# Kernel tuning notes

Hardware: AMD Instinct MI355X
Metric: run time of the kernel (lower is better)

## Reference

```python
import jax, jax.numpy as jnp
import numpy as np

EPS = 1e-6
T = 10.0
STEPS = 3
BN_EPS = 1e-5

def _normalize(x, axis):
    n = jnp.sqrt(jnp.sum(x * x, axis=axis, keepdims=True))
    return x / jnp.maximum(n, EPS)

def _vq_step(X, D):
    # X: (B, d, n), D: (B, d, r)
    Dn = _normalize(D, 1)
    Xn = _normalize(X, 1)
    cos = jnp.einsum('bdr,bdn->brn', Dn, Xn)          # (B, r, n)
    C = jax.nn.softmax(cos / T, axis=1)               # softmax over r
    XCt = jnp.einsum('bdn,brn->bdr', X, C)            # (B, d, r)
    sums = jnp.maximum(jnp.sum(C, axis=2), EPS)       # (B, r)
    D2 = _normalize(XCt / sums[:, None, :], 1)
    Xbar = jnp.einsum('bdr,brn->bdn', D2, C)
    return D2, C, Xbar

def _ham_vq(X, D0):
    # K-1 steps without gradient tracking, final step with grad through X only
    Xs = jax.lax.stop_gradient(X)
    def body(D, _):
        D, _, _ = _vq_step(Xs, D)
        return D, None
    D, _ = jax.lax.scan(body, _normalize(D0, 1), None, length=STEPS - 1)
    D = jax.lax.stop_gradient(D)
    _, _, Xbar = _vq_step(X, D)
    return Xbar

def _conv1x1(x, w, b=None):
    y = jnp.einsum('oc,bchw->bohw', w, x)
    if b is not None:
        y = y + b[None, :, None, None]
    return y

def _bn(x, gamma, beta, mean, var):
    inv = gamma / jnp.sqrt(var + BN_EPS)
    return x * inv[None, :, None, None] + (beta - mean * inv)[None, :, None, None]


def setup_inputs() -> dict:
    key = jax.random.key(0)
    ks = jax.random.split(key, 16)
    B, Cin, H, W = 8, 512, 64, 64
    d_mid, r = 512, 64
    out_ch = 2 * d_mid  # dual
    sc = 0.02
    inp = {
        'z': jax.random.normal(ks[0], (B, Cin, H, W), jnp.float32),
        'lower_w': jax.random.normal(ks[1], (out_ch, Cin), jnp.float32) * sc,
        'lower_b': jnp.zeros((out_ch,), jnp.float32),
        'Dinit_s': jax.random.uniform(ks[2], (B, d_mid, r), jnp.float32),
        'Dinit_c': jax.random.uniform(ks[3], (B, d_mid, r), jnp.float32),
        'cheese_w': jax.random.normal(ks[4], (out_ch, out_ch), jnp.float32) * sc,
        'ch_gamma': jnp.ones((out_ch,), jnp.float32),
        'ch_beta': jnp.zeros((out_ch,), jnp.float32),
        'ch_mean': jax.random.normal(ks[5], (out_ch,), jnp.float32) * 0.1,
        'ch_var': jax.random.uniform(ks[6], (out_ch,), jnp.float32) + 0.5,
        'upper_w': jax.random.normal(ks[7], (Cin, out_ch), jnp.float32) * sc,
        'upper_b': jnp.zeros((Cin,), jnp.float32),
        'h_gamma': jnp.ones((Cin,), jnp.float32),
        'h_beta': jnp.zeros((Cin,), jnp.float32),
        'h_mean': jax.random.normal(ks[8], (Cin,), jnp.float32) * 0.1,
        'h_var': jax.random.uniform(ks[9], (Cin,), jnp.float32) + 0.5,
        'coef_ham': jnp.array(1.0, jnp.float32),
        'coef_shortcut': jnp.array(1.0, jnp.float32),
    }
    return inp


def reference(z, lower_w, lower_b, Dinit_s, Dinit_c, cheese_w,
              ch_gamma, ch_beta, ch_mean, ch_var, upper_w, upper_b,
              h_gamma, h_beta, h_mean, h_var, coef_ham, coef_shortcut):
    B, Cin, H, W = z.shape
    identity = z
    # lower: conv1x1 + relu
    y = jax.nn.relu(_conv1x1(z, lower_w, lower_b))       # (B, 2*d_mid, H, W)
    d_mid = y.shape[1] // 2
    y1, y2 = y[:, :d_mid], y[:, d_mid:]
    n = H * W
    # spatial ham
    Xs = y1.reshape(B, d_mid, n)
    y1 = _ham_vq(Xs, Dinit_s).reshape(B, d_mid, H, W)
    # channel ham (same (B, d, n) flattening; HamMD requires dim1 == d_mid)
    Xc = y2.reshape(B, d_mid, n)
    y2 = _ham_vq(Xc, Dinit_c).reshape(B, d_mid, H, W)
    y = jnp.concatenate([y1, y2], axis=1)
    # cheese: conv1x1(no bias) + BN + relu
    y = jax.nn.relu(_bn(_conv1x1(y, cheese_w), ch_gamma, ch_beta, ch_mean, ch_var))
    # upper conv1x1 + BN
    h = _bn(_conv1x1(y, upper_w, upper_b), h_gamma, h_beta, h_mean, h_var)
    out = coef_ham * h + coef_shortcut * identity
    return jax.nn.relu(out)
```

## Files before the change

kernel.cpp:

```cpp
#include <hip/hip_runtime.h>
#include <hip/hip_bf16.h>

typedef __bf16 bf16_t;
typedef __bf16 bf16x4 __attribute__((ext_vector_type(4)));
typedef __bf16 bf16x8 __attribute__((ext_vector_type(8)));
typedef float  f32x4  __attribute__((ext_vector_type(4)));

#define HEPS 1e-6f

__device__ __forceinline__ void gload16(const bf16_t* g, bf16_t* l) {
    __builtin_amdgcn_global_load_lds(
        (const __attribute__((address_space(1))) unsigned int*)(g),
        (__attribute__((address_space(3))) unsigned int*)(l),
        16, 0, 0);
}


__global__ void cvt_f32_bf16_k(const float* __restrict__ src, bf16_t* __restrict__ dst, int n) {
    int i = blockIdx.x * 256 + threadIdx.x;
    if (i < n) dst[i] = (bf16_t)src[i];
}

__global__ void prep_k(const float* __restrict__ chg, const float* __restrict__ chb,
                       const float* __restrict__ chm, const float* __restrict__ chv,
                       const float* __restrict__ hg, const float* __restrict__ hb,
                       const float* __restrict__ hm, const float* __restrict__ hv,
                       const float* __restrict__ ub, const float* __restrict__ cham,
                       float* __restrict__ chA, float* __restrict__ chB,
                       float* __restrict__ hA2, float* __restrict__ hB2) {
    int i = blockIdx.x * 256 + threadIdx.x;
    if (i < 1024) {
        float inv = chg[i] * rsqrtf(chv[i] + 1e-5f);
        chA[i] = inv;
        chB[i] = chb[i] - chm[i] * inv;
    }
    if (i < 512) {
        float inv = hg[i] * rsqrtf(hv[i] + 1e-5f);
        float cA = cham[0];
        hA2[i] = cA * inv;
        hB2[i] = cA * (fmaf(ub[i], inv, hb[i]) - hm[i] * inv);
    }
}

__global__ void tz_k(const float* __restrict__ z, bf16_t* __restrict__ Zt) {
    __shared__ bf16_t t[64][68];
    int b = blockIdx.z, kt = blockIdx.y, nt = blockIdx.x;
    const float* src = z + ((size_t)b * 512 + kt * 64) * 4096 + nt * 64;
    int tid = threadIdx.x;
    int kr = tid >> 4;
    int nc = (tid & 15) * 4;
    #pragma unroll
    for (int it = 0; it < 4; ++it) {
        int k = kr + it * 16;
        float4 v = *(const float4*)&src[(size_t)k * 4096 + nc];
        t[nc + 0][k] = (bf16_t)v.x; t[nc + 1][k] = (bf16_t)v.y;
        t[nc + 2][k] = (bf16_t)v.z; t[nc + 3][k] = (bf16_t)v.w;
    }
    __syncthreads();
    bf16_t* dst = Zt + ((size_t)b * 4096 + nt * 64) * 512 + kt * 64;
    int nr = tid >> 4;
    int kc = (tid & 15) * 4;
    #pragma unroll
    for (int it = 0; it < 4; ++it) {
        int n = nr + it * 16;
        bf16x4 o;
        #pragma unroll
        for (int c = 0; c < 4; ++c) o[c] = t[n][kc + c];
        *(bf16x4*)&dst[(size_t)n * 512 + kc] = o;
    }
}

__global__ void dinit_k(const float* __restrict__ Ds, const float* __restrict__ Dc,
                        bf16_t* __restrict__ Dt) {
    int bs = blockIdx.y;
    int b = bs >> 1;
    const float* src = ((bs & 1) ? Dc : Ds) + (size_t)b * 512 * 64;
    int idx = blockIdx.x * 256 + threadIdx.x;
    int r = idx & 63, d = idx >> 6;
    Dt[(size_t)bs * 64 * 512 + (size_t)r * 512 + d] = (bf16_t)src[d * 64 + r];
}

__global__ void xnorm2_k(const bf16_t* __restrict__ Xt, float* __restrict__ xinv) {
    int gid = blockIdx.x * 4 + (threadIdx.x >> 6);
    int lane = threadIdx.x & 63;
    int bs = gid >> 12, n = gid & 4095;
    const bf16_t* row = Xt + ((size_t)(bs >> 1) * 4096 + n) * 1024 + (bs & 1) * 512 + lane * 8;
    bf16x8 v = *(const bf16x8*)row;
    float s = 0.f;
    #pragma unroll
    for (int e = 0; e < 8; ++e) { float f = (float)v[e]; s += f * f; }
    #pragma unroll
    for (int off = 32; off > 0; off >>= 1) s += __shfl_xor(s, off);
    if (lane == 0) xinv[gid] = 1.0f / (10.0f * fmaxf(sqrtf(s), HEPS));
}

__global__ void dnorm_k(const bf16_t* __restrict__ Dt, float* __restrict__ dinv) {
    int gw = (blockIdx.x * 256 + threadIdx.x) >> 6;
    int lane = threadIdx.x & 63;
    bf16x8 v = *(const bf16x8*)(Dt + (size_t)gw * 512 + lane * 8);
    float s = 0.f;
    #pragma unroll
    for (int e = 0; e < 8; ++e) { float f = (float)v[e]; s += f * f; }
    #pragma unroll
    for (int off = 32; off > 0; off >>= 1) s += __shfl_xor(s, off);
    if (lane == 0) dinv[gw] = 1.0f / fmaxf(sqrtf(s), HEPS);
}

__global__ void reduce_k(const float* __restrict__ P, bf16_t* __restrict__ Dt,
                         float* __restrict__ dinv) {
    int bsr = blockIdx.x;
    int bs = bsr >> 6, r = bsr & 63;
    int lane = threadIdx.x;
    const float* base = P + ((size_t)(bs * 4) * 64 + r) * 512 + lane * 8;
    float s[8] = {0.f, 0.f, 0.f, 0.f, 0.f, 0.f, 0.f, 0.f};
    #pragma unroll
    for (int kc = 0; kc < 4; ++kc) {
        const float* p = base + (size_t)kc * 64 * 512;
        float4 u = *(const float4*)p;
        float4 w = *(const float4*)(p + 4);
        s[0] += u.x; s[1] += u.y; s[2] += u.z; s[3] += u.w;
        s[4] += w.x; s[5] += w.y; s[6] += w.z; s[7] += w.w;
    }
    bf16x8 o;
    float sq = 0.f;
    #pragma unroll
    for (int e = 0; e < 8; ++e) { sq += s[e] * s[e]; o[e] = (bf16_t)s[e]; }
    *(bf16x8*)&Dt[(size_t)bsr * 512 + lane * 8] = o;
    #pragma unroll
    for (int off = 32; off > 0; off >>= 1) sq += __shfl_xor(sq, off);
    if (lane == 0) dinv[bsr] = 1.0f / fmaxf(sqrtf(sq), HEPS);
}

template<int BM, int BN, int WAVES_M, int WAVES_N, int EPI, int ORDER>
__launch_bounds__(256)
__global__ void g2(const bf16_t* __restrict__ Ag, const bf16_t* __restrict__ Bg,
                   void* __restrict__ Cg, void* __restrict__ C2g,
                   const int M, const int N, const int K,
                   const int ldA, const int ldB, const int ldC,
                   const long aStride, const long bStride,
                   const long cStride, const long c2Stride,
                   const float* __restrict__ p0, const float* __restrict__ p1,
                   const float* __restrict__ scal,
                   const float* __restrict__ shortcut, const long sStride)
{
    constexpr int WM = BM / WAVES_M, WN = BN / WAVES_N;
    constexpr int FM = WM / 16, FN = WN / 16;
    constexpr int ASEG = BM / 64, BSEG = BN / 64;
    constexpr int LPT = ASEG + BSEG;

    __shared__ __align__(64) bf16_t SH[3 * (BM + BN) * 32];
    __shared__ float dl[64];
    bf16_t* Al = SH;
    bf16_t* Bl = SH + 3 * BM * 32;

    const int tid = threadIdx.x;
    const int wave = tid >> 6, lane = tid & 63;
    const int l15 = lane & 15, q = lane >> 4;
    const int lrow = lane >> 2, lcol = (lane & 3) * 8;

    const int gx = gridDim.x, gy = gridDim.y;
    const int per = gx * gy;
    const int nwg = per * gridDim.z;
    const int g = blockIdx.z * per + blockIdx.y * gx + blockIdx.x;
    const int qq = nwg >> 3, rr = nwg & 7;
    const int xcd = g & 7, jj = g >> 3;
    const int w = (xcd < rr ? xcd * (qq + 1) : rr * (qq + 1) + (xcd - rr) * qq) + jj;
    const int bz = w / per;
    const int rem = w - bz * per;
    int bx, by;
    if constexpr (ORDER == 0) { by = rem / gx; bx = rem - by * gx; }
    else                      { bx = rem / gy; by = rem - bx * gy; }

    int bs = bz, exA = 0, exB = 0;
    if constexpr (EPI == 5) { bs = bz >> 2; exA = exB = (bz & 3) * 1024; }
    if constexpr (EPI == 7) { exA = (bz & 1) * 512; }

    const int n0 = bx * BN;
    const int m0 = by * BM;
    const int wm0 = (wave / WAVES_N) * WM;
    const int wn0 = (wave % WAVES_N) * WN;

    const bf16_t* Ab = Ag + (size_t)bs * (size_t)aStride + exA;
    const bf16_t* Bb;
    if constexpr (EPI == 6)
        Bb = Bg + (size_t)(bz >> 1) * (size_t)bStride + (size_t)(bz & 1) * 512;
    else
        Bb = Bg + (size_t)bs * (size_t)bStride + exB;

    if constexpr (EPI == 6) { if (tid < 64) dl[tid] = p0[bz * 64 + tid]; }

    auto stage = [&](int buf, int k0) {
        #pragma unroll
        for (int t = 0; t < ASEG; ++t) {
            int seg = wave * ASEG + t;
            gload16(Ab + (size_t)(m0 + seg * 16 + lrow) * ldA + k0 + lcol,
                    &Al[buf * BM * 32 + seg * 512]);
        }
        #pragma unroll
        for (int t = 0; t < BSEG; ++t) {
            int seg = wave * BSEG + t;
            gload16(Bb + (size_t)(n0 + seg * 16 + lrow) * ldB + k0 + lcol,
                    &Bl[buf * BN * 32 + seg * 512]);
        }
    };

    f32x4 acc[FM][FN];
    #pragma unroll
    for (int i = 0; i < FM; ++i)
        #pragma unroll
        for (int j = 0; j < FN; ++j)
            #pragma unroll
            for (int e = 0; e < 4; ++e) acc[i][j][e] = 0.f;

    const int nK = K / 32;
    stage(0, 0);
    if (nK > 1) stage(1, 32);

    for (int t = 0; t < nK; ++t) {
        const int cur = t % 3;
        if (t + 2 < nK) stage((t + 2) % 3, (t + 2) * 32);

        const int ahead = (nK - 1 - t < 2) ? (nK - 1 - t) : 2;
        if (ahead == 2)      asm volatile("s_waitcnt vmcnt(%0)" :: "i"(2 * LPT) : "memory");
        else if (ahead == 1) asm volatile("s_waitcnt vmcnt(%0)" :: "i"(LPT) : "memory");
        else                 asm volatile("s_waitcnt vmcnt(0)" ::: "memory");
        __builtin_amdgcn_s_barrier();
        __builtin_amdgcn_sched_barrier(0);

        bf16x8 af[FM], bfm[FN];
        #pragma unroll
        for (int i = 0; i < FM; ++i)
            af[i] = *(const bf16x8*)&Al[cur * BM * 32 + (wm0 + 16 * i + l15) * 32 + 8 * q];
        #pragma unroll
        for (int j = 0; j < FN; ++j)
            bfm[j] = *(const bf16x8*)&Bl[cur * BN * 32 + (wn0 + 16 * j + l15) * 32 + 8 * q];

        __builtin_amdgcn_s_setprio(1);
        #pragma unroll
        for (int i = 0; i < FM; ++i)
            #pragma unroll
            for (int j = 0; j < FN; ++j)
                acc[i][j] = __builtin_amdgcn_mfma_f32_16x16x32_bf16(af[i], bfm[j], acc[i][j], 0, 0, 0);
        __builtin_amdgcn_s_setprio(0);

        __builtin_amdgcn_sched_barrier(0);
        __builtin_amdgcn_s_barrier();
    }

    int rowB[FM];
    #pragma unroll
    for (int i = 0; i < FM; ++i) rowB[i] = m0 + wm0 + 16 * i + 4 * q;
    const int colBase = n0 + wn0;

    if constexpr (EPI == 2) {
        bf16_t* O = (bf16_t*)Cg + (size_t)bz * (size_t)cStride;
        #pragma unroll
        for (int j = 0; j < FN; ++j) {
            int col = colBase + 16 * j + l15;
            float a = p0[col], b = p1[col];
            #pragma unroll
            for (int i = 0; i < FM; ++i) {
                int rb = rowB[i];
                #pragma unroll
                for (int e = 0; e < 4; ++e) {
                    float v = fmaxf(fmaf(acc[i][j][e], a, b), 0.f);
                    O[(size_t)(rb + e) * ldC + col] = (bf16_t)v;
                }
            }
        }
    } else if constexpr (EPI == 3) {
        float* O = (float*)Cg + (size_t)bz * (size_t)cStride;
        const float* sc = shortcut + (size_t)bz * (size_t)sStride;
        float cB = scal[0];
        #pragma unroll
        for (int i = 0; i < FM; ++i) {
            int rb = rowB[i];
            #pragma unroll
            for (int e = 0; e < 4; ++e) {
                int row = rb + e;
                float a = p0[row], b = p1[row];
                #pragma unroll
                for (int j = 0; j < FN; ++j) {
                    int col = colBase + 16 * j + l15;
                    float v = fmaf(acc[i][j][e], a, b) + cB * sc[(size_t)row * ldC + col];
                    O[(size_t)row * ldC + col] = fmaxf(v, 0.f);
                }
            }
        }
    } else if constexpr (EPI == 5) {
        float* O = (float*)Cg + (size_t)bz * (size_t)cStride;
        #pragma unroll
        for (int i = 0; i < FM; ++i) {
            int rb = rowB[i];
            #pragma unroll
            for (int j = 0; j < FN; ++j) {
                int col = colBase + 16 * j + l15;
                *(f32x4*)&O[(size_t)col * ldC + rb] = acc[i][j];
            }
        }
    } else if constexpr (EPI == 6) {
        bf16_t* Cc = (bf16_t*)Cg  + (size_t)bz * (size_t)cStride;
        bf16_t* Ct = (bf16_t*)C2g + (size_t)(bz >> 1) * (size_t)c2Stride;
        const int hoff = (bz & 1) * 64;
        const bool doCt = (C2g != nullptr);
        #pragma unroll
        for (int j = 0; j < FN; ++j) {
            int col = colBase + 16 * j + l15;
            float xi = p1[bz * 4096 + col];
            float mx = -1e30f;
            #pragma unroll
            for (int i = 0; i < FM; ++i)
                #pragma unroll
                for (int e = 0; e < 4; ++e) {
                    float v = acc[i][j][e] * dl[rowB[i] + e] * xi;
                    acc[i][j][e] = v;
                    mx = fmaxf(mx, v);
                }
            mx = fmaxf(mx, __shfl_xor(mx, 16));
            mx = fmaxf(mx, __shfl_xor(mx, 32));
            float sm = 0.f;
            #pragma unroll
            for (int i = 0; i < FM; ++i)
                #pragma unroll
                for (int e = 0; e < 4; ++e) {
                    float p = __expf(acc[i][j][e] - mx);
                    acc[i][j][e] = p;
                    sm += p;
                }
            sm += __shfl_xor(sm, 16);
            sm += __shfl_xor(sm, 32);
            float rs = 1.0f / sm;
            #pragma unroll
            for (int i = 0; i < FM; ++i) {
                int rb = rowB[i];
                bf16x4 t;
                #pragma unroll
                for (int e = 0; e < 4; ++e) {
                    t[e] = (bf16_t)(acc[i][j][e] * rs);
                    Cc[(size_t)(rb + e) * ldC + col] = t[e];
                }
                if (doCt) *(bf16x4*)&Ct[(size_t)col * 128 + hoff + rb] = t;
            }
        }
    } else if constexpr (EPI == 7) {
        bf16_t* O = (bf16_t*)Cg + (size_t)(bz >> 1) * (size_t)cStride;
        const int hoff = (bz & 1) * 64;
        #pragma unroll
        for (int j = 0; j < FN; ++j) {
            int col = colBase + 16 * j + l15;
            float di = p0[bz * 64 + col];
            #pragma unroll
            for (int i = 0; i < FM; ++i) {
                int rb = rowB[i];
                #pragma unroll
                for (int e = 0; e < 4; ++e)
                    O[(size_t)(rb + e) * 128 + hoff + col] = (bf16_t)(acc[i][j][e] * di);
            }
        }
    } else if constexpr (EPI == 8) {
        bf16_t* O  = (bf16_t*)Cg  + (size_t)bz * (size_t)cStride;
        bf16_t* O2 = (bf16_t*)C2g + (size_t)bz * (size_t)c2Stride;
        #pragma unroll
        for (int j = 0; j < FN; ++j) {
            int col = colBase + 16 * j + l15;
            float bias = p0[col];
            #pragma unroll
            for (int i = 0; i < FM; ++i) {
                int rb = rowB[i];
                bf16x4 t;
                #pragma unroll
                for (int e = 0; e < 4; ++e) {
                    float v = fmaxf(acc[i][j][e] + bias, 0.f);
                    t[e] = (bf16_t)v;
                    O[(size_t)(rb + e) * ldC + col] = t[e];
                }
                *(bf16x4*)&O2[(size_t)col * 4096 + rb] = t;
            }
        }
    }
}


extern "C" void kernel_launch(void* const* d_in, const int* in_sizes, int n_in,
                              void* d_out, int out_size, void* d_ws, size_t ws_size,
                              hipStream_t stream) {
    const float* z        = (const float*)d_in[0];
    const float* lower_w  = (const float*)d_in[1];
    const float* lower_b  = (const float*)d_in[2];
    const float* Dinit_s  = (const float*)d_in[3];
    const float* Dinit_c  = (const float*)d_in[4];
    const float* cheese_w = (const float*)d_in[5];
    const float* ch_gamma = (const float*)d_in[6];
    const float* ch_beta  = (const float*)d_in[7];
    const float* ch_mean  = (const float*)d_in[8];
    const float* ch_var   = (const float*)d_in[9];
    const float* upper_w  = (const float*)d_in[10];
    const float* upper_b  = (const float*)d_in[11];
    const float* h_gamma  = (const float*)d_in[12];
    const float* h_beta   = (const float*)d_in[13];
    const float* h_mean   = (const float*)d_in[14];
    const float* h_var    = (const float*)d_in[15];
    const float* coef_ham = (const float*)d_in[16];
    const float* coef_sc  = (const float*)d_in[17];

    char* ws = (char*)d_ws;
    size_t off = 0;
    auto alloc = [&](size_t bytes) -> void* {
        void* p = ws + off;
        off += (bytes + 255) & ~(size_t)255;
        return p;
    };

    bf16_t* Wl   = (bf16_t*)alloc((size_t)1024 * 512 * 2);
    bf16_t* Wc   = (bf16_t*)alloc((size_t)1024 * 1024 * 2);
    bf16_t* Wu   = (bf16_t*)alloc((size_t)512 * 1024 * 2);
    float*  chA  = (float*) alloc(1024 * 4);
    float*  chB  = (float*) alloc(1024 * 4);
    float*  hA2  = (float*) alloc(512 * 4);
    float*  hB2  = (float*) alloc(512 * 4);
    float*  dinv = (float*) alloc(1024 * 4);
    float*  xinv = (float*) alloc((size_t)16 * 4096 * 4);
    bf16_t* Xbf  = (bf16_t*)alloc((size_t)8 * 1024 * 4096 * 2);
    bf16_t* Xt   = (bf16_t*)alloc((size_t)8 * 4096 * 1024 * 2);
    bf16_t* Zt   = (bf16_t*)alloc((size_t)8 * 4096 * 512 * 2);
    bf16_t* Cb   = (bf16_t*)alloc((size_t)16 * 64 * 4096 * 2);
    bf16_t* Ct2  = (bf16_t*)alloc((size_t)8 * 4096 * 128 * 2);
    float*  P    = (float*) alloc((size_t)64 * 64 * 512 * 4);
    bf16_t* Dta  = (bf16_t*)alloc((size_t)16 * 64 * 512 * 2);
    bf16_t* Dtb  = (bf16_t*)alloc((size_t)16 * 64 * 512 * 2);
    bf16_t* Eb   = (bf16_t*)alloc((size_t)8 * 1024 * 128 * 2);
    bf16_t* Ycht = Xbf;

    dim3 blk(256);

    cvt_f32_bf16_k<<<2048, blk, 0, stream>>>(lower_w, Wl, 1024 * 512);
    cvt_f32_bf16_k<<<4096, blk, 0, stream>>>(cheese_w, Wc, 1024 * 1024);
    cvt_f32_bf16_k<<<2048, blk, 0, stream>>>(upper_w, Wu, 512 * 1024);
    prep_k<<<4, blk, 0, stream>>>(ch_gamma, ch_beta, ch_mean, ch_var,
                                  h_gamma, h_beta, h_mean, h_var,
                                  upper_b, coef_ham, chA, chB, hA2, hB2);
    tz_k<<<dim3(64, 8, 8), blk, 0, stream>>>(z, Zt);
    dinit_k<<<dim3(128, 16), blk, 0, stream>>>(Dinit_s, Dinit_c, Dta);

    g2<128, 128, 2, 2, 8, 0><<<dim3(8, 32, 8), blk, 0, stream>>>(
        Zt, Wl, (void*)Xt, (void*)Xbf, 4096, 1024, 512,
        512, 512, 1024,
        (long)4096 * 512, 0L, (long)4096 * 1024, (long)1024 * 4096,
        lower_b, nullptr, nullptr, nullptr, 0L);

    xnorm2_k<<<16384, blk, 0, stream>>>(Xt, xinv);
    dnorm_k<<<256, blk, 0, stream>>>(Dta, dinv);

    bf16_t* cur = Dta;
    bf16_t* nxt = Dtb;
    for (int t = 0; t < 3; ++t) {
        g2<64, 256, 1, 4, 6, 0><<<dim3(16, 1, 16), blk, 0, stream>>>(
            cur, Xt, (void*)Cb, (t == 2) ? (void*)Ct2 : nullptr, 64, 4096, 512,
            512, 1024, 4096,
            (long)64 * 512, (long)4096 * 1024, (long)64 * 4096, (long)4096 * 128,
            dinv, xinv, nullptr, nullptr, 0L);
        g2<128, 64, 2, 2, 5, 0><<<dim3(1, 4, 64), blk, 0, stream>>>(
            Xbf, Cb, (void*)P, nullptr, 512, 64, 1024,
            4096, 4096, 512,
            (long)512 * 4096, (long)64 * 4096, (long)64 * 512, 0L,
            nullptr, nullptr, nullptr, nullptr, 0L);
        reduce_k<<<1024, dim3(64), 0, stream>>>(P, nxt, dinv);
        bf16_t* tmp = cur; cur = nxt; nxt = tmp;
    }

    g2<128, 64, 2, 2, 7, 0><<<dim3(1, 8, 16), blk, 0, stream>>>(
        Wc, cur, (void*)Eb, nullptr, 1024, 64, 512,
        1024, 512, 128,
        0L, (long)64 * 512, (long)1024 * 128, 0L,
        dinv, nullptr, nullptr, nullptr, 0L);

    g2<128, 128, 2, 2, 2, 0><<<dim3(8, 32, 8), blk, 0, stream>>>(
        Ct2, Eb, (void*)Ycht, nullptr, 4096, 1024, 128,
        128, 128, 1024,
        (long)4096 * 128, (long)1024 * 128, (long)4096 * 1024, 0L,
        chA, chB, nullptr, nullptr, 0L);

    g2<128, 128, 2, 2, 3, 1><<<dim3(32, 4, 8), blk, 0, stream>>>(
        Wu, Ycht, d_out, nullptr, 512, 4096, 1024,
        1024, 1024, 4096,
        0L, (long)4096 * 1024, (long)512 * 4096, 0L,
        hA2, hB2, coef_sc, z, (long)512 * 4096);

    (void)in_sizes; (void)n_in; (void)out_size; (void)ws_size;
}
```

Baseline: 327.3 us.

## Fuse X column-norm computation into cosine GEMM and restructure pipeline barriers

Removes the separate xnorm2 kernel and its xinv buffer. The cosine GEMM (EPI 6) now accumulates squared X values from the B fragments it already loads and reduces them across lanes in the epilogue. The main loop also moves the wait and barrier to the top of each iteration, before issuing the next stage, and drops the trailing barrier, so there is one barrier per K-step instead of two. The trade is redundant norm recomputation on each of the three VQ iterations and extra VALU work inside the MFMA loop. The new single-barrier ordering must still protect the triple buffer from overwrite.

```diff
diff --git a/kernel.cpp b/kernel.cpp
--- a/kernel.cpp
+++ b/kernel.cpp
@@ -80,20 +80,6 @@
     Dt[(size_t)bs * 64 * 512 + (size_t)r * 512 + d] = (bf16_t)src[d * 64 + r];
 }
 
-__global__ void xnorm2_k(const bf16_t* __restrict__ Xt, float* __restrict__ xinv) {
-    int gid = blockIdx.x * 4 + (threadIdx.x >> 6);
-    int lane = threadIdx.x & 63;
-    int bs = gid >> 12, n = gid & 4095;
-    const bf16_t* row = Xt + ((size_t)(bs >> 1) * 4096 + n) * 1024 + (bs & 1) * 512 + lane * 8;
-    bf16x8 v = *(const bf16x8*)row;
-    float s = 0.f;
-    #pragma unroll
-    for (int e = 0; e < 8; ++e) { float f = (float)v[e]; s += f * f; }
-    #pragma unroll
-    for (int off = 32; off > 0; off >>= 1) s += __shfl_xor(s, off);
-    if (lane == 0) xinv[gid] = 1.0f / (10.0f * fmaxf(sqrtf(s), HEPS));
-}
-
 __global__ void dnorm_k(const bf16_t* __restrict__ Dt, float* __restrict__ dinv) {
     int gw = (blockIdx.x * 256 + threadIdx.x) >> 6;
     int lane = threadIdx.x & 63;
@@ -141,7 +127,7 @@
                    const long cStride, const long c2Stride,
                    const float* __restrict__ p0, const float* __restrict__ p1,
                    const float* __restrict__ scal,
-                   const float* __restrict__ shortcut, const long sStride)
+                   const void* __restrict__ shortcut, const long sStride)
 {
     constexpr int WM = BM / WAVES_M, WN = BN / WAVES_N;
     constexpr int FM = WM / 16, FN = WN / 16;
@@ -212,20 +198,23 @@
             #pragma unroll
             for (int e = 0; e < 4; ++e) acc[i][j][e] = 0.f;
 
+    float xsq[FN];
+    #pragma unroll
+    for (int j = 0; j < FN; ++j) xsq[j] = 0.f;
+
     const int nK = K / 32;
     stage(0, 0);
     if (nK > 1) stage(1, 32);
 
     for (int t = 0; t < nK; ++t) {
         const int cur = t % 3;
+
+        if (t < nK - 1) asm volatile("s_waitcnt vmcnt(%0)" :: "i"(LPT) : "memory");
+        else            asm volatile("s_waitcnt vmcnt(0)" ::: "memory");
+        asm volatile("s_barrier" ::: "memory");
+        __builtin_amdgcn_sched_barrier(0);
+
         if (t + 2 < nK) stage((t + 2) % 3, (t + 2) * 32);
-
-        const int ahead = (nK - 1 - t < 2) ? (nK - 1 - t) : 2;
-        if (ahead == 2)      asm volatile("s_waitcnt vmcnt(%0)" :: "i"(2 * LPT) : "memory");
-        else if (ahead == 1) asm volatile("s_waitcnt vmcnt(%0)" :: "i"(LPT) : "memory");
-        else                 asm volatile("s_waitcnt vmcnt(0)" ::: "memory");
-        __builtin_amdgcn_s_barrier();
-        __builtin_amdgcn_sched_barrier(0);
 
         bf16x8 af[FM], bfm[FN];
         #pragma unroll
@@ -234,6 +223,16 @@
         #pragma unroll
         for (int j = 0; j < FN; ++j)
             bfm[j] = *(const bf16x8*)&Bl[cur * BN * 32 + (wn0 + 16 * j + l15) * 32 + 8 * q];
+
+        if constexpr (EPI == 6) {
+            #pragma unroll
+            for (int j = 0; j < FN; ++j)
+                #pragma unroll
+                for (int e = 0; e < 8; ++e) {
+                    float f = (float)bfm[j][e];
+                    xsq[j] = fmaf(f, f, xsq[j]);
+                }
+        }
 
         __builtin_amdgcn_s_setprio(1);
         #pragma unroll
@@ -242,9 +241,6 @@
             for (int j = 0; j < FN; ++j)
                 acc[i][j] = __builtin_amdgcn_mfma_f32_16x16x32_bf16(af[i], bfm[j], acc[i][j], 0, 0, 0);
         __builtin_amdgcn_s_setprio(0);
-
-        __builtin_amdgcn_sched_barrier(0);
-        __builtin_amdgcn_s_barrier();
     }
 
     int rowB[FM];
@@ -270,7 +266,7 @@
         }
     } else if constexpr (EPI == 3) {
         float* O = (float*)Cg + (size_t)bz * (size_t)cStride;
-        const float* sc = shortcut + (size_t)bz * (size_t)sStride;
+        const float* sc = (const float*)shortcut + (size_t)bz * (size_t)sStride;
         float cB = scal[0];
         #pragma unroll
         for (int i = 0; i < FM; ++i) {
@@ -306,7 +302,10 @@
         #pragma unroll
         for (int j = 0; j < FN; ++j) {
             int col = colBase + 16 * j + l15;
-            float xi = p1[bz * 4096 + col];
+            float s2 = xsq[j];
+            s2 += __shfl_xor(s2, 16);
+            s2 += __shfl_xor(s2, 32);
+            float xi = 1.0f / (10.0f * fmaxf(sqrtf(s2), HEPS));
             float mx = -1e30f;
             #pragma unroll
             for (int i = 0; i < FM; ++i)
@@ -419,7 +418,6 @@
     float*  hA2  = (float*) alloc(512 * 4);
     float*  hB2  = (float*) alloc(512 * 4);
     float*  dinv = (float*) alloc(1024 * 4);
-    float*  xinv = (float*) alloc((size_t)16 * 4096 * 4);
     bf16_t* Xbf  = (bf16_t*)alloc((size_t)8 * 1024 * 4096 * 2);
     bf16_t* Xt   = (bf16_t*)alloc((size_t)8 * 4096 * 1024 * 2);
     bf16_t* Zt   = (bf16_t*)alloc((size_t)8 * 4096 * 512 * 2);
@@ -448,7 +446,6 @@
         (long)4096 * 512, 0L, (long)4096 * 1024, (long)1024 * 4096,
         lower_b, nullptr, nullptr, nullptr, 0L);
 
-    xnorm2_k<<<16384, blk, 0, stream>>>(Xt, xinv);
     dnorm_k<<<256, blk, 0, stream>>>(Dta, dinv);
 
     bf16_t* cur = Dta;
@@ -458,7 +455,7 @@
             cur, Xt, (void*)Cb, (t == 2) ? (void*)Ct2 : nullptr, 64, 4096, 512,
             512, 1024, 4096,
             (long)64 * 512, (long)4096 * 1024, (long)64 * 4096, (long)4096 * 128,
-            dinv, xinv, nullptr, nullptr, 0L);
+            dinv, nullptr, nullptr, nullptr, 0L);
         g2<128, 64, 2, 2, 5, 0><<<dim3(1, 4, 64), blk, 0, stream>>>(
             Xbf, Cb, (void*)P, nullptr, 512, 64, 1024,
             4096, 4096, 512,
```

After: 317.6 us. -3.0%, faster.
